# Performance work log

Measured on AMD Instinct MI355X. Metric: run time of the kernel, lower is better.

Reference implementation:

```python
import jax, jax.numpy as jnp
import numpy as np

B, S, D, H = 64, 512, 1024, 1024

def setup_inputs() -> dict:
    key = jax.random.key(0)
    k1, k2, k3, k4 = jax.random.split(key, 4)
    stdv = 1.0 / np.sqrt(H)
    x = jax.random.normal(k1, (B, S, D), dtype=jnp.float32)
    W = jax.random.uniform(k2, (D, 4 * H), minval=-stdv, maxval=stdv, dtype=jnp.float32)
    U = jax.random.uniform(k3, (H, 4 * H), minval=-stdv, maxval=stdv, dtype=jnp.float32)
    bias = jax.random.uniform(k4, (4 * H,), minval=-stdv, maxval=stdv, dtype=jnp.float32)
    return {"x": x, "W": W, "U": U, "bias": bias}

def reference(x, W, U, bias):
    bs = x.shape[0]
    HS = U.shape[0]
    # Precompute input projections for all timesteps: (S, B, 4H)
    xW = jnp.einsum('bsd,dg->sbg', x, W) + bias

    def step(carry, xw_t):
        h_t, c_t = carry
        gates = xw_t + h_t @ U  # (B, 4H)
        i_t = jax.nn.sigmoid(gates[:, :HS])
        f_t = jax.nn.sigmoid(gates[:, HS:2 * HS])
        g_t = jnp.tanh(gates[:, 2 * HS:3 * HS])
        o_t = jax.nn.sigmoid(gates[:, 3 * HS:])
        c_t = f_t * c_t + i_t * g_t
        h_t = o_t * jnp.tanh(c_t)
        return (h_t, c_t), h_t

    h0 = jnp.zeros((bs, HS), dtype=x.dtype)
    c0 = jnp.zeros((bs, HS), dtype=x.dtype)
    (h_T, c_T), hidden_seq = jax.lax.scan(step, (h0, c0), xW)
    hidden_seq = jnp.transpose(hidden_seq, (1, 0, 2))  # (B, S, H)
    return hidden_seq, (h_T, c_T)
```

## Files before the change

### kernel.cpp

```cpp
#include <hip/hip_runtime.h>
#include <hip/hip_bf16.h>
#include <cstddef>


typedef __attribute__((ext_vector_type(8))) short short8;
typedef __attribute__((ext_vector_type(4))) float f32x4;

static constexpr int Bc = 64, Sc = 512, Dc = 1024, Hc = 1024, G4c = 4096;

__device__ __forceinline__ unsigned short f2bf(float f) {
    unsigned int u = __float_as_uint(f);
    u = u + 0x7FFFu + ((u >> 16) & 1u);
    return (unsigned short)(u >> 16);
}
__device__ __forceinline__ short f2bfs(float f) { return (short)f2bf(f); }
__device__ __forceinline__ float bf2f(unsigned short u) { return __uint_as_float(((unsigned int)u) << 16); }
__device__ __forceinline__ float sigmoidf_(float x) { return 1.0f / (1.0f + __expf(-x)); }
__device__ __forceinline__ float tanhf_(float x) { return 1.0f - 2.0f / (__expf(2.0f * x) + 1.0f); }

__global__ void __launch_bounds__(256) prep_misc(const float* __restrict__ x,
                                                 unsigned short* __restrict__ x16,
                                                 unsigned int* __restrict__ hbufd,
                                                 int n4, int use_x16) {
    const int stride = gridDim.x * 256;
    const int j0 = blockIdx.x * 256 + threadIdx.x;
    for (int k = j0; k < 2 * Bc * Hc; k += stride) hbufd[k] = 0u;
    if (!use_x16) return;
    for (int i = j0; i < n4; i += stride) {
        const float4 v = ((const float4*)x)[i];
        ushort4 o;
        o.x = f2bf(v.x); o.y = f2bf(v.y); o.z = f2bf(v.z); o.w = f2bf(v.w);
        ((ushort4*)x16)[i] = o;
    }
}

__global__ void __launch_bounds__(256) transpose_bf16(const float* __restrict__ src,
                                                      unsigned short* __restrict__ dst) {
    __shared__ unsigned short T[64][72];
    const int kt = blockIdx.x >> 6;
    const int gt = blockIdx.x & 63;
    const int tr = threadIdx.x >> 6;
    const int tc = threadIdx.x & 63;
#pragma unroll
    for (int i = 0; i < 16; ++i) {
        const int r = i * 4 + tr;
        T[tc][r] = f2bf(src[(size_t)(kt * 64 + r) * G4c + gt * 64 + tc]);
    }
    __syncthreads();
#pragma unroll
    for (int i = 0; i < 16; ++i) {
        const int g = i * 4 + tr;
        dst[(size_t)(gt * 64 + g) * 1024 + kt * 64 + tc] = T[g][tc];
    }
}

__global__ void __launch_bounds__(256) gemm_xw(const unsigned short* __restrict__ x16,
                                               const unsigned short* __restrict__ w16t,
                                               void* __restrict__ xw, int mode) {
    const int wg = blockIdx.x;
    const int swz = (wg & 7) * 2048 + (wg >> 3);
    const int nt = swz >> 8;
    const int mt = swz & 255;
    const int w = threadIdx.x >> 6;
    const int lane = threadIdx.x & 63;
    const int q = lane >> 4, l16 = lane & 15;

    const unsigned short* abase = x16 + (size_t)(mt * 128 + w * 16 + l16) * 1024 + q * 8;
    const unsigned short* bbase = w16t + (size_t)(nt * 64 + l16) * 1024 + q * 8;

    f32x4 acc0[4] = {{0,0,0,0},{0,0,0,0},{0,0,0,0},{0,0,0,0}};
    f32x4 acc1[4] = {{0,0,0,0},{0,0,0,0},{0,0,0,0},{0,0,0,0}};
#pragma unroll 4
    for (int kk = 0; kk < 32; ++kk) {
        short8 a0 = *(const short8*)(abase + kk * 32);
        short8 a1 = *(const short8*)(abase + 64 * 1024 + kk * 32);
#pragma unroll
        for (int j = 0; j < 4; ++j) {
            short8 b = *(const short8*)(bbase + (size_t)j * 16 * 1024 + kk * 32);
            acc0[j] = __builtin_amdgcn_mfma_f32_16x16x32_bf16(a0, b, acc0[j], 0, 0, 0);
            acc1[j] = __builtin_amdgcn_mfma_f32_16x16x32_bf16(a1, b, acc1[j], 0, 0, 0);
        }
    }
    const int m0 = mt * 128 + w * 16 + q * 4;
#pragma unroll
    for (int half = 0; half < 2; ++half) {
#pragma unroll
        for (int j = 0; j < 4; ++j)
#pragma unroll
            for (int r = 0; r < 4; ++r) {
                const int m = m0 + half * 64 + r;
                const int b = m >> 9, s = m & 511;
                const size_t o = ((size_t)s * 64 + b) * G4c + nt * 64 + j * 16 + l16;
                const float v = half ? acc1[j][r] : acc0[j][r];
                if (mode == 2) ((float*)xw)[o] = v;
                else ((unsigned short*)xw)[o] = f2bf(v);
            }
    }
}

__global__ void __launch_bounds__(256, 1) lstm_rec(
    const unsigned short* __restrict__ x16, const float* __restrict__ x,
    const unsigned short* __restrict__ w16t, const unsigned short* __restrict__ u16t,
    const float* __restrict__ bias, const void* __restrict__ xw,
    unsigned int* __restrict__ hbufd,
    float* __restrict__ out, int xw_mode, int use_x16) {
    __shared__ short8 hsF[2048];
    __shared__ short8 xsF[2048];
    __shared__ float gbuf[4][16][17];

    const int tid = threadIdx.x;
    const int blk = blockIdx.x >> 6;
    const int cs = blockIdx.x & 63;
    const int col0 = cs * 16;
    const int wv = tid >> 6;
    const int lane = tid & 63;
    const int q = lane >> 4, l16 = lane & 15;
    const int bb = tid >> 4, cc = tid & 15;
    const int gcol = col0 + cc;

    const float bi = bias[gcol], bfv = bias[1024 + gcol], bg = bias[2048 + gcol], bo = bias[3072 + gcol];

    short8 uf[32];
    {
        const unsigned short* ub = u16t + ((size_t)wv * 1024 + col0 + l16) * 1024 + q * 8;
#pragma unroll
        for (int kk = 0; kk < 32; ++kk) uf[kk] = *(const short8*)(ub + kk * 32);
    }
    {
        const short8 z = {0, 0, 0, 0, 0, 0, 0, 0};
#pragma unroll
        for (int i = 0; i < 8; ++i) hsF[i * 256 + tid] = z;
    }
    if (xw_mode == 0) {
#pragma unroll
        for (int i = 0; i < 8; ++i) {
            const int f = i * 256 + tid;
            const int kk = f >> 6, qq = (f >> 4) & 3, b2 = f & 15;
            if (use_x16) {
                const unsigned short* xs = x16 + ((size_t)(blk * 16 + b2) * Sc + 0) * Dc + kk * 32 + qq * 8;
                xsF[f] = *(const short8*)xs;
            } else {
                const float* xs = x + ((size_t)(blk * 16 + b2) * Sc + 0) * Dc + kk * 32 + qq * 8;
                float4 v0 = *(const float4*)xs, v1 = *(const float4*)(xs + 4);
                short8 s;
                s[0] = f2bfs(v0.x); s[1] = f2bfs(v0.y); s[2] = f2bfs(v0.z); s[3] = f2bfs(v0.w);
                s[4] = f2bfs(v1.x); s[5] = f2bfs(v1.y); s[6] = f2bfs(v1.z); s[7] = f2bfs(v1.w);
                xsF[f] = s;
            }
        }
    }
    float pxi = 0.f, pxf = 0.f, pxg = 0.f, pxo = 0.f;
    if (xw_mode == 1) {
        const unsigned short* p = (const unsigned short*)xw + ((size_t)0 * 64 + blk * 16 + bb) * G4c + gcol;
        pxi = bf2f(p[0]); pxf = bf2f(p[1024]); pxg = bf2f(p[2048]); pxo = bf2f(p[3072]);
    } else if (xw_mode == 2) {
        const float* p = (const float*)xw + ((size_t)0 * 64 + blk * 16 + bb) * G4c + gcol;
        pxi = p[0]; pxf = p[1024]; pxg = p[2048]; pxo = p[3072];
    }

    const int kk0 = tid >> 6, qq0 = (tid >> 4) & 3, b20 = tid & 15;

    float c = 0.f;
    for (int t = 0; t < Sc; ++t) {
        __syncthreads();
        f32x4 a0 = {0, 0, 0, 0}, a1 = {0, 0, 0, 0}, a2 = {0, 0, 0, 0}, a3 = {0, 0, 0, 0};
#pragma unroll
        for (int kk = 0; kk < 32; kk += 4) {
            a0 = __builtin_amdgcn_mfma_f32_16x16x32_bf16(hsF[kk * 64 + lane], uf[kk], a0, 0, 0, 0);
            a1 = __builtin_amdgcn_mfma_f32_16x16x32_bf16(hsF[(kk + 1) * 64 + lane], uf[kk + 1], a1, 0, 0, 0);
            a2 = __builtin_amdgcn_mfma_f32_16x16x32_bf16(hsF[(kk + 2) * 64 + lane], uf[kk + 2], a2, 0, 0, 0);
            a3 = __builtin_amdgcn_mfma_f32_16x16x32_bf16(hsF[(kk + 3) * 64 + lane], uf[kk + 3], a3, 0, 0, 0);
        }
        if (xw_mode == 0) {
            const unsigned short* wb = w16t + ((size_t)wv * 1024 + col0 + l16) * 1024 + q * 8;
#pragma unroll
            for (int kk = 0; kk < 32; kk += 4) {
                short8 w0 = *(const short8*)(wb + kk * 32);
                a0 = __builtin_amdgcn_mfma_f32_16x16x32_bf16(xsF[kk * 64 + lane], w0, a0, 0, 0, 0);
                short8 w1 = *(const short8*)(wb + (kk + 1) * 32);
                a1 = __builtin_amdgcn_mfma_f32_16x16x32_bf16(xsF[(kk + 1) * 64 + lane], w1, a1, 0, 0, 0);
                short8 w2 = *(const short8*)(wb + (kk + 2) * 32);
                a2 = __builtin_amdgcn_mfma_f32_16x16x32_bf16(xsF[(kk + 2) * 64 + lane], w2, a2, 0, 0, 0);
                short8 w3 = *(const short8*)(wb + (kk + 3) * 32);
                a3 = __builtin_amdgcn_mfma_f32_16x16x32_bf16(xsF[(kk + 3) * 64 + lane], w3, a3, 0, 0, 0);
            }
        }
#pragma unroll
        for (int r = 0; r < 4; ++r) gbuf[wv][q * 4 + r][l16] = (a0[r] + a1[r]) + (a2[r] + a3[r]);
        __syncthreads();
        float gi = gbuf[0][bb][cc] + pxi + bi;
        float gf = gbuf[1][bb][cc] + pxf + bfv;
        float gg = gbuf[2][bb][cc] + pxg + bg;
        float go = gbuf[3][bb][cc] + pxo + bo;
        gi = sigmoidf_(gi); gf = sigmoidf_(gf); gg = tanhf_(gg); go = sigmoidf_(go);
        c = gf * c + gi * gg;
        const float h = go * tanhf_(c);
        {
            const unsigned int tagv = ((unsigned int)f2bf(h) << 16) | (unsigned int)(t + 1);
            unsigned int* hp = hbufd + (((size_t)(t & 1)) << 16) + (size_t)(blk * 16 + bb) * 1024 + gcol;
            asm volatile("global_store_dword %0, %1, off sc1" :: "v"(hp), "v"(tagv) : "memory");
        }
        out[((size_t)(blk * 16 + bb) * Sc + t) * Hc + gcol] = h;
        if (t == Sc - 1) {
            out[(size_t)Bc * Sc * Hc + (size_t)(blk * 16 + bb) * Hc + gcol] = h;
            out[(size_t)Bc * Sc * Hc + (size_t)Bc * Hc + (size_t)(blk * 16 + bb) * Hc + gcol] = c;
        }
        if (t < Sc - 1) {
            if (xw_mode == 1) {
                const unsigned short* p = (const unsigned short*)xw + ((size_t)(t + 1) * 64 + blk * 16 + bb) * G4c + gcol;
                pxi = bf2f(p[0]); pxf = bf2f(p[1024]); pxg = bf2f(p[2048]); pxo = bf2f(p[3072]);
            } else if (xw_mode == 2) {
                const float* p = (const float*)xw + ((size_t)(t + 1) * 64 + blk * 16 + bb) * G4c + gcol;
                pxi = p[0]; pxf = p[1024]; pxg = p[2048]; pxo = p[3072];
            }
            const unsigned int gen = (unsigned int)(t + 1);
            const unsigned long long genpat = (unsigned long long)gen | ((unsigned long long)gen << 32);
            const unsigned long long* pd = (const unsigned long long*)hbufd +
                (((((size_t)(t & 1)) << 16) + (size_t)(blk * 16 + b20) * 1024 + kk0 * 32 + qq0 * 8) >> 1);
            unsigned long long hv[32];
            for (;;) {
#pragma unroll
                for (int i = 0; i < 8; ++i)
#pragma unroll
                    for (int j = 0; j < 4; ++j)
                        hv[i * 4 + j] = __hip_atomic_load(pd + i * 64 + j, __ATOMIC_RELAXED, __HIP_MEMORY_SCOPE_AGENT);
                unsigned long long bad = 0ull;
#pragma unroll
                for (int i = 0; i < 32; ++i) bad |= (hv[i] ^ genpat) & 0x0000FFFF0000FFFFull;
                if (bad == 0ull) break;
                __builtin_amdgcn_s_sleep(1);
            }
#pragma unroll
            for (int i = 0; i < 8; ++i) {
                short8 s;
                unsigned int* sp = (unsigned int*)&s;
#pragma unroll
                for (int j = 0; j < 4; ++j) {
                    const unsigned long long v = hv[i * 4 + j];
                    sp[j] = ((unsigned int)(v >> 16) & 0xFFFFu) | ((unsigned int)(v >> 32) & 0xFFFF0000u);
                }
                hsF[i * 256 + tid] = s;
            }
            if (xw_mode == 0) {
#pragma unroll
                for (int i = 0; i < 8; ++i) {
                    const int f = i * 256 + tid;
                    const int kk = f >> 6, qq = (f >> 4) & 3, b2 = f & 15;
                    if (use_x16) {
                        const unsigned short* xs = x16 + ((size_t)(blk * 16 + b2) * Sc + (t + 1)) * Dc + kk * 32 + qq * 8;
                        xsF[f] = *(const short8*)xs;
                    } else {
                        const float* xs = x + ((size_t)(blk * 16 + b2) * Sc + (t + 1)) * Dc + kk * 32 + qq * 8;
                        float4 v0 = *(const float4*)xs, v1 = *(const float4*)(xs + 4);
                        short8 s;
                        s[0] = f2bfs(v0.x); s[1] = f2bfs(v0.y); s[2] = f2bfs(v0.z); s[3] = f2bfs(v0.w);
                        s[4] = f2bfs(v1.x); s[5] = f2bfs(v1.y); s[6] = f2bfs(v1.z); s[7] = f2bfs(v1.w);
                        xsF[f] = s;
                    }
                }
            }
        }
    }
}

extern "C" void kernel_launch(void* const* d_in, const int* in_sizes, int n_in,
                              void* d_out, int out_size, void* d_ws, size_t ws_size,
                              hipStream_t stream) {
    const float* x = (const float*)d_in[0];
    const float* W = (const float*)d_in[1];
    const float* U = (const float*)d_in[2];
    const float* bias = (const float*)d_in[3];
    float* out = (float*)d_out;

    char* wsb = (char*)d_ws;
    unsigned int* hbufd = (unsigned int*)wsb;
    unsigned short* u16t = (unsigned short*)(wsb + 524288);
    unsigned short* w16t = (unsigned short*)(wsb + 524288 + 8388608);
    unsigned short* x16 = (unsigned short*)(wsb + 17301504);
    void* xw = (void*)(wsb + 84410368);

    const size_t base = 84410368ull;
    const size_t need1 = base + 268435456ull;
    const size_t need2 = base + 536870912ull;

    int xw_mode, use_x16;
    if (ws_size >= need2)      { xw_mode = 2; use_x16 = 1; }
    else if (ws_size >= need1) { xw_mode = 1; use_x16 = 1; }
    else if (ws_size >= base)  { xw_mode = 0; use_x16 = 1; }
    else                       { xw_mode = 0; use_x16 = 0; }

    const int n4 = (Bc * Sc * Dc) / 4;
    hipLaunchKernelGGL(prep_misc, dim3(2048), dim3(256), 0, stream, x, x16, hbufd, n4, use_x16);
    hipLaunchKernelGGL(transpose_bf16, dim3(1024), dim3(256), 0, stream, U, u16t);
    hipLaunchKernelGGL(transpose_bf16, dim3(1024), dim3(256), 0, stream, W, w16t);
    if (xw_mode >= 1)
        hipLaunchKernelGGL(gemm_xw, dim3(16384), dim3(256), 0, stream, x16, w16t, xw, xw_mode);
    hipLaunchKernelGGL(lstm_rec, dim3(256), dim3(256), 0, stream,
                       x16, x, w16t, u16t, bias, xw, hbufd, out, xw_mode, use_x16);
}
```

Before: 4.734 ms.

## Repartition LSTM recurrence: 512-thread blocks over 8 batch rows and 32 columns

Each persistent block now handles 8 batch rows and 32 hidden columns with 512 threads (8 waves), instead of 16 rows and 16 columns with 256 threads. Shared memory becomes dynamic. Each thread now polls only 8 qwords of the tagged h buffer instead of 32, which is meant to cut per-step synchronisation latency. The MFMA tiles are half empty because only 8 of the 16 rows are real, the elementwise work is masked so only half the threads do it, and a guard counter is added to the spin-wait loop.

```diff
diff --git a/kernel.cpp b/kernel.cpp
--- a/kernel.cpp
+++ b/kernel.cpp
@@ -20,11 +20,11 @@
 
 __global__ void __launch_bounds__(256) prep_misc(const float* __restrict__ x,
                                                  unsigned short* __restrict__ x16,
-                                                 unsigned int* __restrict__ hbufd,
-                                                 int n4, int use_x16) {
+                                                 unsigned int* __restrict__ hbufs,
+                                                 int nz, int n4, int use_x16) {
     const int stride = gridDim.x * 256;
     const int j0 = blockIdx.x * 256 + threadIdx.x;
-    for (int k = j0; k < 2 * Bc * Hc; k += stride) hbufd[k] = 0u;
+    for (int k = j0; k < nz; k += stride) hbufs[k] = 0u;
     if (!use_x16) return;
     for (int i = j0; i < n4; i += stride) {
         const float4 v = ((const float4*)x)[i];
@@ -98,67 +98,79 @@
     }
 }
 
-__global__ void __launch_bounds__(256, 1) lstm_rec(
+__global__ void __launch_bounds__(512, 2) lstm_rec(
     const unsigned short* __restrict__ x16, const float* __restrict__ x,
     const unsigned short* __restrict__ w16t, const unsigned short* __restrict__ u16t,
     const float* __restrict__ bias, const void* __restrict__ xw,
-    unsigned int* __restrict__ hbufd,
+    unsigned int* __restrict__ hbufs,
     float* __restrict__ out, int xw_mode, int use_x16) {
-    __shared__ short8 hsF[2048];
-    __shared__ short8 xsF[2048];
-    __shared__ float gbuf[4][16][17];
+    extern __shared__ char smem[];
+    short8* hsF = (short8*)smem;
+    float (*gbuf)[4][16][17] = (float (*)[4][16][17])(smem + 32768);
+    short8* xsF = (short8*)(smem + 41472);
 
     const int tid = threadIdx.x;
-    const int blk = blockIdx.x >> 6;
-    const int cs = blockIdx.x & 63;
-    const int col0 = cs * 16;
+    const int bid = blockIdx.x;
+    const int blk = bid & 7;
+    const int cs = bid >> 3;
+    const int col0 = cs * 32;
     const int wv = tid >> 6;
     const int lane = tid & 63;
     const int q = lane >> 4, l16 = lane & 15;
-    const int bb = tid >> 4, cc = tid & 15;
+    const int g = wv & 3;
+    const int cs2 = wv >> 2;
+    const int bb = tid >> 5, cc = tid & 31;
     const int gcol = col0 + cc;
+    const bool actE = (bb < 8);
+    const int b3 = tid & 7, u6 = tid >> 3;
 
     const float bi = bias[gcol], bfv = bias[1024 + gcol], bg = bias[2048 + gcol], bo = bias[3072 + gcol];
 
     short8 uf[32];
     {
-        const unsigned short* ub = u16t + ((size_t)wv * 1024 + col0 + l16) * 1024 + q * 8;
+        const unsigned short* ub = u16t + ((size_t)(g * 1024 + col0 + cs2 * 16 + l16)) * 1024 + q * 8;
 #pragma unroll
         for (int kk = 0; kk < 32; ++kk) uf[kk] = *(const short8*)(ub + kk * 32);
     }
     {
         const short8 z = {0, 0, 0, 0, 0, 0, 0, 0};
 #pragma unroll
-        for (int i = 0; i < 8; ++i) hsF[i * 256 + tid] = z;
+        for (int i = 0; i < 4; ++i) hsF[i * 512 + tid] = z;
+        if (xw_mode == 0) {
+#pragma unroll
+            for (int i = 0; i < 4; ++i) xsF[i * 512 + tid] = z;
+        }
     }
     if (xw_mode == 0) {
 #pragma unroll
-        for (int i = 0; i < 8; ++i) {
-            const int f = i * 256 + tid;
+        for (int i = 0; i < 4; ++i) {
+            const int f = i * 512 + tid;
             const int kk = f >> 6, qq = (f >> 4) & 3, b2 = f & 15;
-            if (use_x16) {
-                const unsigned short* xs = x16 + ((size_t)(blk * 16 + b2) * Sc + 0) * Dc + kk * 32 + qq * 8;
-                xsF[f] = *(const short8*)xs;
-            } else {
-                const float* xs = x + ((size_t)(blk * 16 + b2) * Sc + 0) * Dc + kk * 32 + qq * 8;
-                float4 v0 = *(const float4*)xs, v1 = *(const float4*)(xs + 4);
-                short8 s;
-                s[0] = f2bfs(v0.x); s[1] = f2bfs(v0.y); s[2] = f2bfs(v0.z); s[3] = f2bfs(v0.w);
-                s[4] = f2bfs(v1.x); s[5] = f2bfs(v1.y); s[6] = f2bfs(v1.z); s[7] = f2bfs(v1.w);
-                xsF[f] = s;
+            if (b2 < 8) {
+                if (use_x16) {
+                    const unsigned short* xs = x16 + ((size_t)(blk * 8 + b2) * Sc + 0) * Dc + kk * 32 + qq * 8;
+                    xsF[f] = *(const short8*)xs;
+                } else {
+                    const float* xs = x + ((size_t)(blk * 8 + b2) * Sc + 0) * Dc + kk * 32 + qq * 8;
+                    float4 v0 = *(const float4*)xs, v1 = *(const float4*)(xs + 4);
+                    short8 s;
+                    s[0] = f2bfs(v0.x); s[1] = f2bfs(v0.y); s[2] = f2bfs(v0.z); s[3] = f2bfs(v0.w);
+                    s[4] = f2bfs(v1.x); s[5] = f2bfs(v1.y); s[6] = f2bfs(v1.z); s[7] = f2bfs(v1.w);
+                    xsF[f] = s;
+                }
             }
         }
     }
     float pxi = 0.f, pxf = 0.f, pxg = 0.f, pxo = 0.f;
-    if (xw_mode == 1) {
-        const unsigned short* p = (const unsigned short*)xw + ((size_t)0 * 64 + blk * 16 + bb) * G4c + gcol;
-        pxi = bf2f(p[0]); pxf = bf2f(p[1024]); pxg = bf2f(p[2048]); pxo = bf2f(p[3072]);
-    } else if (xw_mode == 2) {
-        const float* p = (const float*)xw + ((size_t)0 * 64 + blk * 16 + bb) * G4c + gcol;
-        pxi = p[0]; pxf = p[1024]; pxg = p[2048]; pxo = p[3072];
-    }
-
-    const int kk0 = tid >> 6, qq0 = (tid >> 4) & 3, b20 = tid & 15;
+    if (actE) {
+        if (xw_mode == 1) {
+            const unsigned short* p = (const unsigned short*)xw + ((size_t)0 * 64 + blk * 8 + bb) * G4c + gcol;
+            pxi = bf2f(p[0]); pxf = bf2f(p[1024]); pxg = bf2f(p[2048]); pxo = bf2f(p[3072]);
+        } else if (xw_mode == 2) {
+            const float* p = (const float*)xw + ((size_t)0 * 64 + blk * 8 + bb) * G4c + gcol;
+            pxi = p[0]; pxf = p[1024]; pxg = p[2048]; pxo = p[3072];
+        }
+    }
 
     float c = 0.f;
     for (int t = 0; t < Sc; ++t) {
@@ -172,7 +184,7 @@
             a3 = __builtin_amdgcn_mfma_f32_16x16x32_bf16(hsF[(kk + 3) * 64 + lane], uf[kk + 3], a3, 0, 0, 0);
         }
         if (xw_mode == 0) {
-            const unsigned short* wb = w16t + ((size_t)wv * 1024 + col0 + l16) * 1024 + q * 8;
+            const unsigned short* wb = w16t + ((size_t)(g * 1024 + col0 + cs2 * 16 + l16)) * 1024 + q * 8;
 #pragma unroll
             for (int kk = 0; kk < 32; kk += 4) {
                 short8 w0 = *(const short8*)(wb + kk * 32);
@@ -186,76 +198,80 @@
             }
         }
 #pragma unroll
-        for (int r = 0; r < 4; ++r) gbuf[wv][q * 4 + r][l16] = (a0[r] + a1[r]) + (a2[r] + a3[r]);
+        for (int r = 0; r < 4; ++r) gbuf[cs2][g][q * 4 + r][l16] = (a0[r] + a1[r]) + (a2[r] + a3[r]);
         __syncthreads();
-        float gi = gbuf[0][bb][cc] + pxi + bi;
-        float gf = gbuf[1][bb][cc] + pxf + bfv;
-        float gg = gbuf[2][bb][cc] + pxg + bg;
-        float go = gbuf[3][bb][cc] + pxo + bo;
-        gi = sigmoidf_(gi); gf = sigmoidf_(gf); gg = tanhf_(gg); go = sigmoidf_(go);
-        c = gf * c + gi * gg;
-        const float h = go * tanhf_(c);
-        {
+        if (actE) {
+            const int ch = cc >> 4, c16 = cc & 15;
+            float gi = gbuf[ch][0][bb][c16] + pxi + bi;
+            float gf = gbuf[ch][1][bb][c16] + pxf + bfv;
+            float gg = gbuf[ch][2][bb][c16] + pxg + bg;
+            float go = gbuf[ch][3][bb][c16] + pxo + bo;
+            gi = sigmoidf_(gi); gf = sigmoidf_(gf); gg = tanhf_(gg); go = sigmoidf_(go);
+            c = gf * c + gi * gg;
+            const float h = go * tanhf_(c);
             const unsigned int tagv = ((unsigned int)f2bf(h) << 16) | (unsigned int)(t + 1);
-            unsigned int* hp = hbufd + (((size_t)(t & 1)) << 16) + (size_t)(blk * 16 + bb) * 1024 + gcol;
+            unsigned int* hp = hbufs + (((size_t)(t & 1)) << 16) + (size_t)(blk * 8 + bb) * 1024 + gcol;
             asm volatile("global_store_dword %0, %1, off sc1" :: "v"(hp), "v"(tagv) : "memory");
-        }
-        out[((size_t)(blk * 16 + bb) * Sc + t) * Hc + gcol] = h;
-        if (t == Sc - 1) {
-            out[(size_t)Bc * Sc * Hc + (size_t)(blk * 16 + bb) * Hc + gcol] = h;
-            out[(size_t)Bc * Sc * Hc + (size_t)Bc * Hc + (size_t)(blk * 16 + bb) * Hc + gcol] = c;
+            out[((size_t)(blk * 8 + bb) * Sc + t) * Hc + gcol] = h;
+            if (t == Sc - 1) {
+                out[(size_t)Bc * Sc * Hc + (size_t)(blk * 8 + bb) * Hc + gcol] = h;
+                out[(size_t)Bc * Sc * Hc + (size_t)Bc * Hc + (size_t)(blk * 8 + bb) * Hc + gcol] = c;
+            }
         }
         if (t < Sc - 1) {
-            if (xw_mode == 1) {
-                const unsigned short* p = (const unsigned short*)xw + ((size_t)(t + 1) * 64 + blk * 16 + bb) * G4c + gcol;
-                pxi = bf2f(p[0]); pxf = bf2f(p[1024]); pxg = bf2f(p[2048]); pxo = bf2f(p[3072]);
-            } else if (xw_mode == 2) {
-                const float* p = (const float*)xw + ((size_t)(t + 1) * 64 + blk * 16 + bb) * G4c + gcol;
-                pxi = p[0]; pxf = p[1024]; pxg = p[2048]; pxo = p[3072];
+            if (actE) {
+                if (xw_mode == 1) {
+                    const unsigned short* p = (const unsigned short*)xw + ((size_t)(t + 1) * 64 + blk * 8 + bb) * G4c + gcol;
+                    pxi = bf2f(p[0]); pxf = bf2f(p[1024]); pxg = bf2f(p[2048]); pxo = bf2f(p[3072]);
+                } else if (xw_mode == 2) {
+                    const float* p = (const float*)xw + ((size_t)(t + 1) * 64 + blk * 8 + bb) * G4c + gcol;
+                    pxi = p[0]; pxf = p[1024]; pxg = p[2048]; pxo = p[3072];
+                }
             }
             const unsigned int gen = (unsigned int)(t + 1);
             const unsigned long long genpat = (unsigned long long)gen | ((unsigned long long)gen << 32);
-            const unsigned long long* pd = (const unsigned long long*)hbufd +
-                (((((size_t)(t & 1)) << 16) + (size_t)(blk * 16 + b20) * 1024 + kk0 * 32 + qq0 * 8) >> 1);
-            unsigned long long hv[32];
+            const unsigned long long* pd = (const unsigned long long*)hbufs +
+                (((((size_t)(t & 1)) << 16) + (size_t)(blk * 8 + b3) * 1024 + u6 * 16) >> 1);
+            unsigned long long hv[8];
+            int guard = 0;
             for (;;) {
 #pragma unroll
-                for (int i = 0; i < 8; ++i)
-#pragma unroll
-                    for (int j = 0; j < 4; ++j)
-                        hv[i * 4 + j] = __hip_atomic_load(pd + i * 64 + j, __ATOMIC_RELAXED, __HIP_MEMORY_SCOPE_AGENT);
+                for (int j = 0; j < 8; ++j)
+                    hv[j] = __hip_atomic_load(pd + j, __ATOMIC_RELAXED, __HIP_MEMORY_SCOPE_AGENT);
                 unsigned long long bad = 0ull;
 #pragma unroll
-                for (int i = 0; i < 32; ++i) bad |= (hv[i] ^ genpat) & 0x0000FFFF0000FFFFull;
-                if (bad == 0ull) break;
+                for (int j = 0; j < 8; ++j) bad |= (hv[j] ^ genpat) & 0x0000FFFF0000FFFFull;
+                if (bad == 0ull || ++guard > (1 << 16)) break;
                 __builtin_amdgcn_s_sleep(1);
             }
 #pragma unroll
-            for (int i = 0; i < 8; ++i) {
+            for (int half = 0; half < 2; ++half) {
                 short8 s;
                 unsigned int* sp = (unsigned int*)&s;
 #pragma unroll
-                for (int j = 0; j < 4; ++j) {
-                    const unsigned long long v = hv[i * 4 + j];
-                    sp[j] = ((unsigned int)(v >> 16) & 0xFFFFu) | ((unsigned int)(v >> 32) & 0xFFFF0000u);
+                for (int w = 0; w < 4; ++w) {
+                    const unsigned long long v = hv[half * 4 + w];
+                    sp[w] = ((unsigned int)(v >> 16) & 0xFFFFu) | ((unsigned int)(v >> 32) & 0xFFFF0000u);
                 }
-                hsF[i * 256 + tid] = s;
+                hsF[(u6 >> 1) * 64 + ((u6 & 1) * 2 + half) * 16 + b3] = s;
             }
             if (xw_mode == 0) {
 #pragma unroll
-                for (int i = 0; i < 8; ++i) {
-                    const int f = i * 256 + tid;
+                for (int i = 0; i < 4; ++i) {
+                    const int f = i * 512 + tid;
                     const int kk = f >> 6, qq = (f >> 4) & 3, b2 = f & 15;
-                    if (use_x16) {
-                        const unsigned short* xs = x16 + ((size_t)(blk * 16 + b2) * Sc + (t + 1)) * Dc + kk * 32 + qq * 8;
-                        xsF[f] = *(const short8*)xs;
-                    } else {
-                        const float* xs = x + ((size_t)(blk * 16 + b2) * Sc + (t + 1)) * Dc + kk * 32 + qq * 8;
-                        float4 v0 = *(const float4*)xs, v1 = *(const float4*)(xs + 4);
-                        short8 s;
-                        s[0] = f2bfs(v0.x); s[1] = f2bfs(v0.y); s[2] = f2bfs(v0.z); s[3] = f2bfs(v0.w);
-                        s[4] = f2bfs(v1.x); s[5] = f2bfs(v1.y); s[6] = f2bfs(v1.z); s[7] = f2bfs(v1.w);
-                        xsF[f] = s;
+                    if (b2 < 8) {
+                        if (use_x16) {
+                            const unsigned short* xs = x16 + ((size_t)(blk * 8 + b2) * Sc + (t + 1)) * Dc + kk * 32 + qq * 8;
+                            xsF[f] = *(const short8*)xs;
+                        } else {
+                            const float* xs = x + ((size_t)(blk * 8 + b2) * Sc + (t + 1)) * Dc + kk * 32 + qq * 8;
+                            float4 v0 = *(const float4*)xs, v1 = *(const float4*)(xs + 4);
+                            short8 s;
+                            s[0] = f2bfs(v0.x); s[1] = f2bfs(v0.y); s[2] = f2bfs(v0.z); s[3] = f2bfs(v0.w);
+                            s[4] = f2bfs(v1.x); s[5] = f2bfs(v1.y); s[6] = f2bfs(v1.z); s[7] = f2bfs(v1.w);
+                            xsF[f] = s;
+                        }
                     }
                 }
             }
@@ -273,9 +289,9 @@
     float* out = (float*)d_out;
 
     char* wsb = (char*)d_ws;
-    unsigned int* hbufd = (unsigned int*)wsb;
+    unsigned int* hbufs = (unsigned int*)wsb;
     unsigned short* u16t = (unsigned short*)(wsb + 524288);
-    unsigned short* w16t = (unsigned short*)(wsb + 524288 + 8388608);
+    unsigned short* w16t = (unsigned short*)(wsb + 8912896);
     unsigned short* x16 = (unsigned short*)(wsb + 17301504);
     void* xw = (void*)(wsb + 84410368);
 
@@ -290,11 +306,17 @@
     else                       { xw_mode = 0; use_x16 = 0; }
 
     const int n4 = (Bc * Sc * Dc) / 4;
-    hipLaunchKernelGGL(prep_misc, dim3(2048), dim3(256), 0, stream, x, x16, hbufd, n4, use_x16);
+    const int nz = 524288 / 4;
+    hipLaunchKernelGGL(prep_misc, dim3(2048), dim3(256), 0, stream, x, x16, hbufs, nz, n4, use_x16);
     hipLaunchKernelGGL(transpose_bf16, dim3(1024), dim3(256), 0, stream, U, u16t);
     hipLaunchKernelGGL(transpose_bf16, dim3(1024), dim3(256), 0, stream, W, w16t);
     if (xw_mode >= 1)
         hipLaunchKernelGGL(gemm_xw, dim3(16384), dim3(256), 0, stream, x16, w16t, xw, xw_mode);
-    hipLaunchKernelGGL(lstm_rec, dim3(256), dim3(256), 0, stream,
-                       x16, x, w16t, u16t, bias, xw, hbufd, out, xw_mode, use_x16);
-}
+
+    const unsigned int shmem = (xw_mode == 0) ? 74240u : 41472u;
+    if (xw_mode == 0)
+        hipFuncSetAttribute((const void*)lstm_rec, hipFuncAttributeMaxDynamicSharedMemorySize, 74240);
+
+    hipLaunchKernelGGL(lstm_rec, dim3(256), dim3(512), shmem, stream,
+                       x16, x, w16t, u16t, bias, xw, hbufs, out, xw_mode, use_x16);
+}
```

Measured after the change: 5.541 ms. +17.0%, slower.
